# Performance work log

Measured on AMD Instinct MI355X. Metric: run time of the kernel, lower is better.

## Reference

```python
import jax, jax.numpy as jnp
import numpy as np

B = 65536       # number of segments (molecules/graphs) = max(batch_indices[0]) + 1
N = 1048576     # nodes per eye
IN_NF, R_OUT, C_OUT = 64, 128, 128
BRAIN_IN, BRAIN_H, BRAIN_OUT = 256, 256, 128


def setup_inputs() -> dict:
    key = jax.random.key(0)
    ks = jax.random.split(key, 16)
    f = jax.random.normal
    s_in = 1.0 / np.sqrt(IN_NF)
    s_r = 1.0 / np.sqrt(R_OUT)
    s_b = 1.0 / np.sqrt(BRAIN_IN)
    s_h = 1.0 / np.sqrt(BRAIN_H)
    return {
        "x0": f(ks[0], (N, IN_NF), jnp.float32),
        "x1": f(ks[1], (N, IN_NF), jnp.float32),
        "idx0": jax.random.randint(ks[2], (N,), 0, B, dtype=jnp.int32),
        "idx1": jax.random.randint(ks[3], (N,), 0, B, dtype=jnp.int32),
        "Wr0": f(ks[4], (IN_NF, R_OUT), jnp.float32) * s_in,
        "br0": jnp.zeros((R_OUT,), jnp.float32),
        "Wc0": f(ks[5], (R_OUT, C_OUT), jnp.float32) * s_r,
        "bc0": jnp.zeros((C_OUT,), jnp.float32),
        "Wr1": f(ks[6], (IN_NF, R_OUT), jnp.float32) * s_in,
        "br1": jnp.zeros((R_OUT,), jnp.float32),
        "Wc1": f(ks[7], (R_OUT, C_OUT), jnp.float32) * s_r,
        "bc1": jnp.zeros((C_OUT,), jnp.float32),
        "Wb1": f(ks[8], (BRAIN_IN, BRAIN_H), jnp.float32) * s_b,
        "bb1": jnp.zeros((BRAIN_H,), jnp.float32),
        "Wb2": f(ks[9], (BRAIN_H, BRAIN_OUT), jnp.float32) * s_h,
        "bb2": jnp.zeros((BRAIN_OUT,), jnp.float32),
    }


def _eye(x, idx, Wr, br, Wc, bc):
    # linear + relu per node: [N, r_out]
    h = jax.nn.relu(x @ Wr + br)
    # scatter-mean over segments -> [B, r_out]; empty segments get 0 (matches
    # torch_scatter mean and the original zero-padding up to maxlen)
    s = jax.ops.segment_sum(h, idx, num_segments=B)
    cnt = jax.ops.segment_sum(jnp.ones((h.shape[0],), h.dtype), idx, num_segments=B)
    mean = s / jnp.maximum(cnt, 1.0)[:, None]
    # per-graph linear + relu -> [B, c_out]
    return jax.nn.relu(mean @ Wc + bc)


def reference(x0, x1, idx0, idx1, Wr0, br0, Wc0, bc0, Wr1, br1, Wc1, bc1, Wb1, bb1, Wb2, bb2):
    e0 = _eye(x0, idx0, Wr0, br0, Wc0, bc0)   # [B, 128]
    e1 = _eye(x1, idx1, Wr1, br1, Wc1, bc1)   # [B, 128]
    z = jnp.concatenate([e0, e1], axis=1)      # [B, 256]
    h = jax.nn.relu(z @ Wb1 + bb1)             # [B, 256]
    return h @ Wb2 + bb2                       # [B, 128]
```

## Files before the change

### kernel.cpp

```cpp
#include <hip/hip_runtime.h>
#include <hip/hip_bf16.h>

#define B_SEG 65536
#define N_NODES 1048576

typedef _Float16 f16;
typedef __attribute__((ext_vector_type(8))) _Float16 f16x8;
typedef __attribute__((ext_vector_type(2))) __fp16 fp16x2;
typedef __attribute__((ext_vector_type(4))) float f32x4;

union F16x8 { f16x8 v; fp16x2 h2[4]; };

#define MFMA16(a, b, acc) __builtin_amdgcn_mfma_f32_16x16x32_f16((a), (b), (acc), 0, 0, 0)

__global__ __launch_bounds__(256) void histo_part(const int* __restrict__ idx0,
        const int* __restrict__ idx1, int* __restrict__ cnt0, int* __restrict__ cnt1) {
    int part  = blockIdx.x & 7;
    int chunk = blockIdx.x >> 3;
    int base  = chunk * (N_NODES / 256);
    for (int i = base + threadIdx.x; i < base + N_NODES / 256; i += 256) {
        int s0 = idx0[i];
        if ((s0 >> 13) == part) atomicAdd(&cnt0[s0], 1);
        int s1 = idx1[i];
        if ((s1 >> 13) == part) atomicAdd(&cnt1[s1], 1);
    }
}

__global__ __launch_bounds__(256) void scan1(const int* __restrict__ cnt, int* __restrict__ bsum) {
    int b = blockIdx.x, t = threadIdx.x;
    int4 v = ((const int4*)cnt)[b * 256 + t];
    int s = v.x + v.y + v.z + v.w;
    for (int d = 1; d < 64; d <<= 1) s += __shfl_xor(s, d);
    __shared__ int ws4[4];
    if ((t & 63) == 0) ws4[t >> 6] = s;
    __syncthreads();
    if (t == 0) bsum[b] = ws4[0] + ws4[1] + ws4[2] + ws4[3];
}

__global__ __launch_bounds__(128) void scan2(int* __restrict__ bsum) {
    int t = threadIdx.x, lane = t & 63;
    int v = bsum[t];
    int s = v;
    for (int d = 1; d < 64; d <<= 1) { int u = __shfl_up(s, d); if (lane >= d) s += u; }
    bsum[t] = s - v;
}

__global__ __launch_bounds__(256) void scan3(int* __restrict__ cnt, const int* __restrict__ bsum,
                                             int* __restrict__ off0, int* __restrict__ off1) {
    int b = blockIdx.x, t = threadIdx.x;
    int4 v = ((const int4*)cnt)[b * 256 + t];
    int local = v.x + v.y + v.z + v.w;
    int lane = t & 63, w = t >> 6;
    int s = local;
    for (int d = 1; d < 64; d <<= 1) { int u = __shfl_up(s, d); if (lane >= d) s += u; }
    __shared__ int wsum[4];
    if (lane == 63) wsum[w] = s;
    __syncthreads();
    int carry = bsum[b];
    for (int i = 0; i < w; ++i) carry += wsum[i];
    int ex = carry + s - local;
    int* off = (b < 64) ? off0 : off1;
    int gi = (b & 63) * 1024 + t * 4;
    off[gi] = ex; ex += v.x; off[gi + 1] = ex; ex += v.y; off[gi + 2] = ex; ex += v.z; off[gi + 3] = ex;
    int4 z; z.x = 0; z.y = 0; z.z = 0; z.w = 0;
    ((int4*)cnt)[b * 256 + t] = z;
    if (b == 0 && t == 0) { off0[B_SEG] = N_NODES; off1[B_SEG] = N_NODES; }
}

__global__ __launch_bounds__(256) void fill_part(const int* __restrict__ idx0,
        const int* __restrict__ idx1, const int* __restrict__ off0, const int* __restrict__ off1,
        int* __restrict__ cur0, int* __restrict__ cur1,
        int* __restrict__ ord0, int* __restrict__ ord1) {
    int part  = blockIdx.x & 7;
    int chunk = blockIdx.x >> 3;
    int base  = chunk * (N_NODES / 256);
    for (int i = base + threadIdx.x; i < base + N_NODES / 256; i += 256) {
        int s0 = idx0[i];
        if ((s0 >> 13) == part) { int p = atomicAdd(&cur0[s0], 1); ord0[off0[s0] + p] = i; }
        int s1 = idx1[i];
        if ((s1 >> 13) == part) { int p = atomicAdd(&cur1[s1], 1); ord1[off1[s1] + p] = i; }
    }
}

__global__ __launch_bounds__(256) void prep_weights(
        const float* __restrict__ Wc0, const float* __restrict__ Wc1,
        const float* __restrict__ Wb1, const float* __restrict__ Wb2,
        f16* __restrict__ T0, f16* __restrict__ T1, f16* __restrict__ T2, f16* __restrict__ T3) {
    int b = blockIdx.x, t = threadIdx.x;
    if (b < 64)        { int i = b * 256 + t;         T0[i] = (f16)Wc0[(i & 127) * 128 + (i >> 7)]; }
    else if (b < 128)  { int i = (b - 64) * 256 + t;  T1[i] = (f16)Wc1[(i & 127) * 128 + (i >> 7)]; }
    else if (b < 384)  { int i = (b - 128) * 256 + t; T2[i] = (f16)Wb1[(i & 255) * 256 + (i >> 8)]; }
    else               { int i = (b - 384) * 256 + t; T3[i] = (f16)Wb2[(i & 255) * 128 + (i >> 8)]; }
}

#define SEGS_PER_WAVE 8
__global__ __launch_bounds__(256, 3) void eye_means_mfma(
        const float* __restrict__ xA, const float* __restrict__ WrA, const float* __restrict__ brA,
        const int* __restrict__ offA, const int* __restrict__ ordA, f16* __restrict__ meansA,
        const float* __restrict__ xB, const float* __restrict__ WrB, const float* __restrict__ brB,
        const int* __restrict__ offB, const int* __restrict__ ordB, f16* __restrict__ meansB) {
    const float *x, *Wr, *br; const int *off, *ord; f16* means;
    if (blockIdx.y == 0) { x = xA; Wr = WrA; br = brA; off = offA; ord = ordA; means = meansA; }
    else                 { x = xB; Wr = WrB; br = brB; off = offB; ord = ordB; means = meansB; }

    int lane = threadIdx.x & 63;
    int wid  = blockIdx.x * 4 + (threadIdx.x >> 6);
    int c  = lane & 15;
    int kq = lane >> 4;

    f16x8 bfr[8][2];
    float rbias[8];
    #pragma unroll
    for (int g = 0; g < 8; ++g) {
        #pragma unroll
        for (int h = 0; h < 2; ++h)
            #pragma unroll
            for (int j = 0; j < 8; ++j)
                bfr[g][h][j] = (f16)Wr[(size_t)(h * 32 + kq * 8 + j) * 128 + g * 16 + c];
        rbias[g] = br[g * 16 + c];
    }

    int s_begin = wid * SEGS_PER_WAVE;
    int offv  = off[s_begin + ((lane <= 8) ? lane : 8)];
    int base0 = __shfl(offv, 0);
    int nxtv  = __shfl(offv, (lane < 8) ? (lane + 1) : 8);
    int szl   = nxtv - offv;

    int ov0 = ord[base0 + lane];
    int ov1 = ord[base0 + 64 + lane];
    int ov2 = ord[base0 + 128 + lane];

    auto node_at = [&](int off_rel, int sz, int r) -> int {
        int e  = off_rel + r;
        int e6 = e & 63;
        int n0 = __shfl(ov0, e6);
        int n1 = __shfl(ov1, e6);
        int n2 = __shfl(ov2, e6);
        int n  = (e < 64) ? n0 : (e < 128) ? n1 : n2;
        if (e >= 192) n = ord[base0 + e];
        return (r < sz) ? n : 0;
    };

    auto loadx = [&](int node, float4& v0, float4& v1, float4& v2, float4& v3) {
        const float* xp = &x[(size_t)node * 64 + kq * 8];
        v0 = *(const float4*)(xp);      v1 = *(const float4*)(xp + 4);
        v2 = *(const float4*)(xp + 32); v3 = *(const float4*)(xp + 36);
    };

    float sum[8];
    #pragma unroll
    for (int g = 0; g < 8; ++g) sum[g] = 0.f;

    float4 ca, cb, cc, cd;
    {
        int sz0 = __shfl(szl, 0);
        loadx(node_at(0, sz0, c), ca, cb, cc, cd);
    }

    #pragma unroll
    for (int s = 0; s < SEGS_PER_WAVE; ++s) {
        int off_rel   = __shfl(offv, s) - base0;
        int sz        = __shfl(szl, s);
        int nb        = (sz + 15) >> 4;
        int off_rel_n = (s < SEGS_PER_WAVE - 1) ? (__shfl(offv, s + 1) - base0) : 0;
        int sz_n      = (s < SEGS_PER_WAVE - 1) ? __shfl(szl, s + 1) : 0;
        size_t mb     = (size_t)(s_begin + s) * 128;

        if (nb == 0) {
            means[mb + (2 * kq + 0) * 16 + c] = (f16)0.f;
            means[mb + (2 * kq + 1) * 16 + c] = (f16)0.f;
            loadx(node_at(off_rel_n, sz_n, c), ca, cb, cc, cd);
            continue;
        }

        for (int b = 0; b < nb; ++b) {
            int nn = (b + 1 < nb) ? node_at(off_rel, sz, (b + 1) * 16 + c)
                                  : node_at(off_rel_n, sz_n, c);
            float4 pa, pb, pc, pd;
            loadx(nn, pa, pb, pc, pd);

            f16x8 A0 = {}, A1 = {};
            if (b * 16 + c < sz) {
                F16x8 u0, u1;
                u0.h2[0] = __builtin_amdgcn_cvt_pkrtz(ca.x, ca.y);
                u0.h2[1] = __builtin_amdgcn_cvt_pkrtz(ca.z, ca.w);
                u0.h2[2] = __builtin_amdgcn_cvt_pkrtz(cb.x, cb.y);
                u0.h2[3] = __builtin_amdgcn_cvt_pkrtz(cb.z, cb.w);
                u1.h2[0] = __builtin_amdgcn_cvt_pkrtz(cc.x, cc.y);
                u1.h2[1] = __builtin_amdgcn_cvt_pkrtz(cc.z, cc.w);
                u1.h2[2] = __builtin_amdgcn_cvt_pkrtz(cd.x, cd.y);
                u1.h2[3] = __builtin_amdgcn_cvt_pkrtz(cd.z, cd.w);
                A0 = u0.v; A1 = u1.v;
            }
            #pragma unroll
            for (int g = 0; g < 8; ++g) {
                f32x4 acc = {0.f, 0.f, 0.f, 0.f};
                acc = MFMA16(A0, bfr[g][0], acc);
                acc = MFMA16(A1, bfr[g][1], acc);
                #pragma unroll
                for (int r = 0; r < 4; ++r)
                    sum[g] += fmaxf(acc[r] + rbias[g], 0.f);
            }
            ca = pa; cb = pb; cc = pc; cd = pd;
        }

        float padc = (float)(nb * 16 - sz);
        float inv  = 1.f / (float)sz;
        #pragma unroll
        for (int g = 0; g < 8; ++g) {
            float v = sum[g];
            v += __shfl_xor(v, 16);
            v += __shfl_xor(v, 32);
            v -= padc * fmaxf(rbias[g], 0.f);
            sum[g] = v * inv;
        }
        means[mb + (2 * kq + 0) * 16 + c] = (f16)sum[2 * kq + 0];
        means[mb + (2 * kq + 1) * 16 + c] = (f16)sum[2 * kq + 1];
        #pragma unroll
        for (int g = 0; g < 8; ++g) sum[g] = 0.f;
    }
}

template<int K, int RELU, int OUT16>
__global__ __launch_bounds__(256) void gemm16(
        const f16* __restrict__ A, const f16* __restrict__ BT,
        const float* __restrict__ bias, void* __restrict__ Cv, int ldc) {
    int lane = threadIdx.x & 63;
    int w = threadIdx.x >> 6;
    int c = lane & 15, kq = lane >> 4;
    int m0 = blockIdx.x * 128 + w * 32;
    int n0 = blockIdx.y * 128;

    f32x4 acc[2][8] = {};
    const f16* arow0 = A + (size_t)(m0 + c) * K + kq * 8;
    const f16* arow1 = arow0 + (size_t)16 * K;
    const f16* brow  = BT + (size_t)(n0 + c) * K + kq * 8;

    #pragma unroll 2
    for (int k0 = 0; k0 < K; k0 += 32) {
        f16x8 a0 = *(const f16x8*)(arow0 + k0);
        f16x8 a1 = *(const f16x8*)(arow1 + k0);
        #pragma unroll
        for (int g = 0; g < 8; ++g) {
            f16x8 bf = *(const f16x8*)(brow + (size_t)g * 16 * K + k0);
            acc[0][g] = MFMA16(a0, bf, acc[0][g]);
            acc[1][g] = MFMA16(a1, bf, acc[1][g]);
        }
    }

    #pragma unroll
    for (int g = 0; g < 8; ++g) {
        float bv = bias[n0 + g * 16 + c];
        #pragma unroll
        for (int ms = 0; ms < 2; ++ms) {
            #pragma unroll
            for (int r = 0; r < 4; ++r) {
                float v = acc[ms][g][r] + bv;
                if (RELU) v = fmaxf(v, 0.f);
                size_t ci = (size_t)(m0 + ms * 16 + kq * 4 + r) * ldc + n0 + g * 16 + c;
                if (OUT16) ((f16*)Cv)[ci] = (f16)v;
                else       ((float*)Cv)[ci] = v;
            }
        }
    }
}

extern "C" void kernel_launch(void* const* d_in, const int* in_sizes, int n_in,
                              void* d_out, int out_size, void* d_ws, size_t ws_size,
                              hipStream_t stream) {
    const float* x0  = (const float*)d_in[0];
    const float* x1  = (const float*)d_in[1];
    const int*   idx0 = (const int*)d_in[2];
    const int*   idx1 = (const int*)d_in[3];
    const float* Wr0 = (const float*)d_in[4];
    const float* br0 = (const float*)d_in[5];
    const float* Wc0 = (const float*)d_in[6];
    const float* bc0 = (const float*)d_in[7];
    const float* Wr1 = (const float*)d_in[8];
    const float* br1 = (const float*)d_in[9];
    const float* Wc1 = (const float*)d_in[10];
    const float* bc1 = (const float*)d_in[11];
    const float* Wb1 = (const float*)d_in[12];
    const float* bb1 = (const float*)d_in[13];
    const float* Wb2 = (const float*)d_in[14];
    const float* bb2 = (const float*)d_in[15];
    float* out = (float*)d_out;

    char* w = (char*)d_ws;
    auto alloc = [&](size_t bytes) { void* p = (void*)w; w += (bytes + 255) & ~(size_t)255; return p; };
    int* cnt0 = (int*)alloc((size_t)B_SEG * 4);
    int* cnt1 = (int*)alloc((size_t)B_SEG * 4);
    int* off0 = (int*)alloc((size_t)(B_SEG + 1) * 4);
    int* off1 = (int*)alloc((size_t)(B_SEG + 1) * 4);
    int* ord0 = (int*)alloc((size_t)(N_NODES + 256) * 4);
    int* ord1 = (int*)alloc((size_t)(N_NODES + 256) * 4);
    int* bsum = (int*)alloc(128 * 4);
    f16* means0 = (f16*)alloc((size_t)B_SEG * 128 * 2);
    f16* means1 = (f16*)alloc((size_t)B_SEG * 128 * 2);
    f16* z      = (f16*)alloc((size_t)B_SEG * 256 * 2);
    f16* hb     = (f16*)alloc((size_t)B_SEG * 256 * 2);
    f16* T0     = (f16*)alloc((size_t)128 * 128 * 2);
    f16* T1     = (f16*)alloc((size_t)128 * 128 * 2);
    f16* T2     = (f16*)alloc((size_t)256 * 256 * 2);
    f16* T3     = (f16*)alloc((size_t)128 * 256 * 2);

    (void)hipMemsetAsync(cnt0, 0, 2 * (size_t)B_SEG * sizeof(int), stream);
    histo_part<<<2048, 256, 0, stream>>>(idx0, idx1, cnt0, cnt1);
    scan1<<<128, 256, 0, stream>>>(cnt0, bsum);
    scan2<<<1, 128, 0, stream>>>(bsum);
    scan3<<<128, 256, 0, stream>>>(cnt0, bsum, off0, off1);
    fill_part<<<2048, 256, 0, stream>>>(idx0, idx1, off0, off1, cnt0, cnt1, ord0, ord1);
    prep_weights<<<512, 256, 0, stream>>>(Wc0, Wc1, Wb1, Wb2, T0, T1, T2, T3);

    eye_means_mfma<<<dim3(2048, 2), 256, 0, stream>>>(
        x0, Wr0, br0, off0, ord0, means0,
        x1, Wr1, br1, off1, ord1, means1);

    gemm16<128, 1, 1><<<dim3(512, 1), 256, 0, stream>>>(means0, T0, bc0, z,       256);
    gemm16<128, 1, 1><<<dim3(512, 1), 256, 0, stream>>>(means1, T1, bc1, z + 128, 256);
    gemm16<256, 1, 1><<<dim3(512, 2), 256, 0, stream>>>(z,  T2, bb1, hb,  256);
    gemm16<256, 0, 0><<<dim3(512, 1), 256, 0, stream>>>(hb, T3, bb2, out, 128);
}
```

Measured before the change: 466.2 us.

## Record per-node ranks during histogram and fuse both per-eye Wc GEMMs

```diff
diff --git a/kernel.cpp b/kernel.cpp
--- a/kernel.cpp
+++ b/kernel.cpp
@@ -8,21 +8,23 @@
 typedef __attribute__((ext_vector_type(8))) _Float16 f16x8;
 typedef __attribute__((ext_vector_type(2))) __fp16 fp16x2;
 typedef __attribute__((ext_vector_type(4))) float f32x4;
+typedef unsigned short u16;
 
 union F16x8 { f16x8 v; fp16x2 h2[4]; };
 
 #define MFMA16(a, b, acc) __builtin_amdgcn_mfma_f32_16x16x32_f16((a), (b), (acc), 0, 0, 0)
 
 __global__ __launch_bounds__(256) void histo_part(const int* __restrict__ idx0,
-        const int* __restrict__ idx1, int* __restrict__ cnt0, int* __restrict__ cnt1) {
+        const int* __restrict__ idx1, int* __restrict__ cnt0, int* __restrict__ cnt1,
+        u16* __restrict__ rank0, u16* __restrict__ rank1) {
     int part  = blockIdx.x & 7;
     int chunk = blockIdx.x >> 3;
     int base  = chunk * (N_NODES / 256);
     for (int i = base + threadIdx.x; i < base + N_NODES / 256; i += 256) {
         int s0 = idx0[i];
-        if ((s0 >> 13) == part) atomicAdd(&cnt0[s0], 1);
+        if ((s0 >> 13) == part) { int p = atomicAdd(&cnt0[s0], 1); rank0[i] = (u16)p; }
         int s1 = idx1[i];
-        if ((s1 >> 13) == part) atomicAdd(&cnt1[s1], 1);
+        if ((s1 >> 13) == part) { int p = atomicAdd(&cnt1[s1], 1); rank1[i] = (u16)p; }
     }
 }
 
@@ -45,7 +47,7 @@
     bsum[t] = s - v;
 }
 
-__global__ __launch_bounds__(256) void scan3(int* __restrict__ cnt, const int* __restrict__ bsum,
+__global__ __launch_bounds__(256) void scan3(const int* __restrict__ cnt, const int* __restrict__ bsum,
                                              int* __restrict__ off0, int* __restrict__ off1) {
     int b = blockIdx.x, t = threadIdx.x;
     int4 v = ((const int4*)cnt)[b * 256 + t];
@@ -62,23 +64,17 @@
     int* off = (b < 64) ? off0 : off1;
     int gi = (b & 63) * 1024 + t * 4;
     off[gi] = ex; ex += v.x; off[gi + 1] = ex; ex += v.y; off[gi + 2] = ex; ex += v.z; off[gi + 3] = ex;
-    int4 z; z.x = 0; z.y = 0; z.z = 0; z.w = 0;
-    ((int4*)cnt)[b * 256 + t] = z;
     if (b == 0 && t == 0) { off0[B_SEG] = N_NODES; off1[B_SEG] = N_NODES; }
 }
 
-__global__ __launch_bounds__(256) void fill_part(const int* __restrict__ idx0,
-        const int* __restrict__ idx1, const int* __restrict__ off0, const int* __restrict__ off1,
-        int* __restrict__ cur0, int* __restrict__ cur1,
+__global__ __launch_bounds__(256) void fill_simple(const int* __restrict__ idx0,
+        const int* __restrict__ idx1, const u16* __restrict__ rank0, const u16* __restrict__ rank1,
+        const int* __restrict__ off0, const int* __restrict__ off1,
         int* __restrict__ ord0, int* __restrict__ ord1) {
-    int part  = blockIdx.x & 7;
-    int chunk = blockIdx.x >> 3;
-    int base  = chunk * (N_NODES / 256);
-    for (int i = base + threadIdx.x; i < base + N_NODES / 256; i += 256) {
-        int s0 = idx0[i];
-        if ((s0 >> 13) == part) { int p = atomicAdd(&cur0[s0], 1); ord0[off0[s0] + p] = i; }
-        int s1 = idx1[i];
-        if ((s1 >> 13) == part) { int p = atomicAdd(&cur1[s1], 1); ord1[off1[s1] + p] = i; }
+    int stride = gridDim.x * blockDim.x;
+    for (int i = blockIdx.x * blockDim.x + threadIdx.x; i < N_NODES; i += stride) {
+        ord0[off0[idx0[i]] + rank0[i]] = i;
+        ord1[off1[idx1[i]] + rank1[i]] = i;
     }
 }
 
@@ -265,6 +261,51 @@
     }
 }
 
+__global__ __launch_bounds__(256) void gemm_wc(
+        const f16* __restrict__ M0, const f16* __restrict__ M1,
+        const f16* __restrict__ T0, const f16* __restrict__ T1,
+        const float* __restrict__ bc0, const float* __restrict__ bc1,
+        f16* __restrict__ z) {
+    int e = blockIdx.y;
+    const f16* A  = e ? M1 : M0;
+    const f16* BT = e ? T1 : T0;
+    const float* bias = e ? bc1 : bc0;
+    int lane = threadIdx.x & 63;
+    int w = threadIdx.x >> 6;
+    int c = lane & 15, kq = lane >> 4;
+    int m0 = blockIdx.x * 128 + w * 32;
+
+    f32x4 acc[2][8] = {};
+    const f16* arow0 = A + (size_t)(m0 + c) * 128 + kq * 8;
+    const f16* arow1 = arow0 + (size_t)16 * 128;
+    const f16* brow  = BT + (size_t)c * 128 + kq * 8;
+
+    #pragma unroll
+    for (int k0 = 0; k0 < 128; k0 += 32) {
+        f16x8 a0 = *(const f16x8*)(arow0 + k0);
+        f16x8 a1 = *(const f16x8*)(arow1 + k0);
+        #pragma unroll
+        for (int g = 0; g < 8; ++g) {
+            f16x8 bf = *(const f16x8*)(brow + (size_t)g * 16 * 128 + k0);
+            acc[0][g] = MFMA16(a0, bf, acc[0][g]);
+            acc[1][g] = MFMA16(a1, bf, acc[1][g]);
+        }
+    }
+
+    #pragma unroll
+    for (int g = 0; g < 8; ++g) {
+        float bv = bias[g * 16 + c];
+        #pragma unroll
+        for (int ms = 0; ms < 2; ++ms) {
+            #pragma unroll
+            for (int r = 0; r < 4; ++r) {
+                float v = fmaxf(acc[ms][g][r] + bv, 0.f);
+                z[(size_t)(m0 + ms * 16 + kq * 4 + r) * 256 + e * 128 + g * 16 + c] = (f16)v;
+            }
+        }
+    }
+}
+
 extern "C" void kernel_launch(void* const* d_in, const int* in_sizes, int n_in,
                               void* d_out, int out_size, void* d_ws, size_t ws_size,
                               hipStream_t stream) {
@@ -294,6 +335,8 @@
     int* off1 = (int*)alloc((size_t)(B_SEG + 1) * 4);
     int* ord0 = (int*)alloc((size_t)(N_NODES + 256) * 4);
     int* ord1 = (int*)alloc((size_t)(N_NODES + 256) * 4);
+    u16* rank0 = (u16*)alloc((size_t)N_NODES * 2);
+    u16* rank1 = (u16*)alloc((size_t)N_NODES * 2);
     int* bsum = (int*)alloc(128 * 4);
     f16* means0 = (f16*)alloc((size_t)B_SEG * 128 * 2);
     f16* means1 = (f16*)alloc((size_t)B_SEG * 128 * 2);
@@ -305,19 +348,18 @@
     f16* T3     = (f16*)alloc((size_t)128 * 256 * 2);
 
     (void)hipMemsetAsync(cnt0, 0, 2 * (size_t)B_SEG * sizeof(int), stream);
-    histo_part<<<2048, 256, 0, stream>>>(idx0, idx1, cnt0, cnt1);
+    histo_part<<<2048, 256, 0, stream>>>(idx0, idx1, cnt0, cnt1, rank0, rank1);
     scan1<<<128, 256, 0, stream>>>(cnt0, bsum);
     scan2<<<1, 128, 0, stream>>>(bsum);
     scan3<<<128, 256, 0, stream>>>(cnt0, bsum, off0, off1);
-    fill_part<<<2048, 256, 0, stream>>>(idx0, idx1, off0, off1, cnt0, cnt1, ord0, ord1);
+    fill_simple<<<2048, 256, 0, stream>>>(idx0, idx1, rank0, rank1, off0, off1, ord0, ord1);
     prep_weights<<<512, 256, 0, stream>>>(Wc0, Wc1, Wb1, Wb2, T0, T1, T2, T3);
 
     eye_means_mfma<<<dim3(2048, 2), 256, 0, stream>>>(
         x0, Wr0, br0, off0, ord0, means0,
         x1, Wr1, br1, off1, ord1, means1);
 
-    gemm16<128, 1, 1><<<dim3(512, 1), 256, 0, stream>>>(means0, T0, bc0, z,       256);
-    gemm16<128, 1, 1><<<dim3(512, 1), 256, 0, stream>>>(means1, T1, bc1, z + 128, 256);
+    gemm_wc<<<dim3(512, 2), 256, 0, stream>>>(means0, means1, T0, T1, bc0, bc1, z);
     gemm16<256, 1, 1><<<dim3(512, 2), 256, 0, stream>>>(z,  T2, bb1, hb,  256);
     gemm16<256, 0, 0><<<dim3(512, 1), 256, 0, stream>>>(hb, T3, bb2, out, 128);
 }
```

Result: faster. 421.4 us (-9.6%).
